# Performance work log

Measured on AMD Instinct MI355X. Metric: run time of the kernel, lower is better.

Reference implementation:

```python
import jax, jax.numpy as jnp
import numpy as np

N_NODES = 50000
N_EDGES = 800000
N_FEAT = 256
HIDDEN = 64
N_CLASSES = 16
T_END = 3.0  # opt['time']; rk4 takes one step over [0, 3]


def spline_conv(x, src, dst, p, W, R, b, n):
    """SplineConv, dim=1, kernel_size=2, degree=1 open B-spline, aggr='mean'.
    x: [n, Cin]; src/dst: [E]; p: [E,1] pseudo-coords in [0,1];
    W: [2, Cin, Cout]; R: [Cin, Cout]; b: [Cout]."""
    xj = x[src]  # gather source node features [E, Cin]
    # basis weights for K=2, degree=1: (1-p) on kernel 0, p on kernel 1
    msg = ((1.0 - p) * xj) @ W[0] + (p * xj) @ W[1]  # [E, Cout]
    agg = jax.ops.segment_sum(msg, dst, num_segments=n)
    deg = jax.ops.segment_sum(jnp.ones((msg.shape[0], 1), msg.dtype), dst, num_segments=n)
    return agg / jnp.maximum(deg, 1.0) + x @ R + b


def setup_inputs() -> dict:
    key = jax.random.key(0)
    ks = jax.random.split(key, 20)
    x = jax.random.normal(ks[0], (N_NODES, N_FEAT), jnp.float32)
    edge_attr = jax.random.uniform(ks[1], (N_EDGES, 1), jnp.float32)
    src = jax.random.randint(ks[2], (N_EDGES,), 0, N_NODES)
    dst = jax.random.randint(ks[3], (N_EDGES,), 0, N_NODES)

    def w(k, shape, fan_in):
        s = 1.0 / np.sqrt(fan_in)
        return jax.random.uniform(k, shape, jnp.float32, -s, s)

    # conv1: num_features -> hidden
    W1 = w(ks[4], (2, N_FEAT, HIDDEN), N_FEAT)
    R1 = w(ks[5], (N_FEAT, HIDDEN), N_FEAT)
    b1 = jnp.zeros((HIDDEN,), jnp.float32)
    # ODE func: two stacked SplineConvs hidden -> hidden
    Wa = w(ks[6], (2, HIDDEN, HIDDEN), HIDDEN)
    Ra = w(ks[7], (HIDDEN, HIDDEN), HIDDEN)
    ba = jnp.zeros((HIDDEN,), jnp.float32)
    Wb = w(ks[8], (2, HIDDEN, HIDDEN), HIDDEN)
    Rb = w(ks[9], (HIDDEN, HIDDEN), HIDDEN)
    bb = jnp.zeros((HIDDEN,), jnp.float32)
    # conv2: hidden -> num_classes
    W2 = w(ks[10], (2, HIDDEN, N_CLASSES), HIDDEN)
    R2 = w(ks[11], (HIDDEN, N_CLASSES), HIDDEN)
    b2 = jnp.zeros((N_CLASSES,), jnp.float32)

    return dict(x=x, edge_attr=edge_attr, src=src, dst=dst,
                W1=W1, R1=R1, b1=b1, Wa=Wa, Ra=Ra, ba=ba,
                Wb=Wb, Rb=Rb, bb=bb, W2=W2, R2=R2, b2=b2)


def reference(x, edge_attr, src, dst, W1, R1, b1, Wa, Ra, ba, Wb, Rb, bb, W2, R2, b2):
    n = x.shape[0]
    p = edge_attr
    h = jnp.tanh(spline_conv(x, src, dst, p, W1, R1, b1, n))
    # dropout is identity in eval mode

    def f(y):  # GCNLayer: two stacked SplineConvs, no activation
        y = spline_conv(y, src, dst, p, Wa, Ra, ba, n)
        return spline_conv(y, src, dst, p, Wb, Rb, bb, n)

    # single RK4 step from t=0 to t=T_END (torchdiffeq fixed-grid rk4 on s_span=[0,3])
    k1 = f(h)
    k2 = f(h + 0.5 * T_END * k1)
    k3 = f(h + 0.5 * T_END * k2)
    k4 = f(h + T_END * k3)
    h = h + (T_END / 6.0) * (k1 + 2.0 * k2 + 2.0 * k3 + k4)

    out = jnp.tanh(spline_conv(h, src, dst, p, W2, R2, b2, n))
    return jax.nn.log_softmax(out, axis=1)
```

## Files before the change

### kernel.cpp

```cpp
#include <hip/hip_runtime.h>
#include <math.h>

static inline int ceil_div(int a, int b) { return (a + b - 1) / b; }


__global__ __launch_bounds__(256) void zero2(int* __restrict__ a, int* __restrict__ b,
                                             int n) {
    int i = blockIdx.x * 256 + threadIdx.x;
    if (i < n) { a[i] = 0; b[i] = 0; }
}

__global__ __launch_bounds__(256) void hist_kernel(const int* __restrict__ dst,
                                                   int* __restrict__ deg, int E) {
    int e = blockIdx.x * 256 + threadIdx.x;
    if (e < E) atomicAdd(&deg[dst[e]], 1);
}

__global__ __launch_bounds__(256) void scan_blocksum(const int* __restrict__ deg,
                                                     int* __restrict__ bsum, int n) {
    __shared__ int red[256];
    int t = threadIdx.x;
    int base = blockIdx.x * 2048 + t * 8;
    int s = 0;
    #pragma unroll
    for (int i = 0; i < 8; ++i) {
        int idx = base + i;
        if (idx < n) s += deg[idx];
    }
    red[t] = s;
    __syncthreads();
    #pragma unroll
    for (int off = 128; off >= 1; off >>= 1) {
        if (t < off) red[t] += red[t + off];
        __syncthreads();
    }
    if (t == 0) bsum[blockIdx.x] = red[0];
}

__global__ __launch_bounds__(256) void scan_tops(int* __restrict__ bsum, int nb) {
    __shared__ int sh[256];
    int t = threadIdx.x;
    int orig = (t < nb) ? bsum[t] : 0;
    sh[t] = orig;
    __syncthreads();
    for (int off = 1; off < 256; off <<= 1) {
        int add = (t >= off) ? sh[t - off] : 0;
        __syncthreads();
        sh[t] += add;
        __syncthreads();
    }
    if (t < nb) bsum[t] = sh[t] - orig;
}

__global__ __launch_bounds__(256) void scan_final(const int* __restrict__ deg,
                                                  const int* __restrict__ bsum,
                                                  int* __restrict__ rowp,
                                                  float* __restrict__ invd,
                                                  int n, int E) {
    __shared__ int sh[256];
    int t = threadIdx.x;
    int base = blockIdx.x * 2048 + t * 8;
    int loc[8];
    int s = 0;
    #pragma unroll
    for (int i = 0; i < 8; ++i) {
        int idx = base + i;
        int d = (idx < n) ? deg[idx] : 0;
        loc[i] = d;
        s += d;
    }
    sh[t] = s;
    __syncthreads();
    for (int off = 1; off < 256; off <<= 1) {
        int add = (t >= off) ? sh[t - off] : 0;
        __syncthreads();
        sh[t] += add;
        __syncthreads();
    }
    int run = bsum[blockIdx.x] + (sh[t] - s);
    #pragma unroll
    for (int i = 0; i < 8; ++i) {
        int idx = base + i;
        if (idx < n) {
            rowp[idx] = run;
            int d = loc[i];
            run += d;
            invd[idx] = 1.0f / (float)(d > 1 ? d : 1);
        }
    }
    if (blockIdx.x == 0 && t == 0) rowp[n] = E;
}

__global__ __launch_bounds__(256) void scatter_idx(const int* __restrict__ dst,
                                                   const int* __restrict__ rowp,
                                                   int* __restrict__ fill,
                                                   int* __restrict__ ei, int E) {
    int e = blockIdx.x * 256 + threadIdx.x;
    if (e >= E) return;
    int d = dst[e];
    int pos = rowp[d] + atomicAdd(&fill[d], 1);
    ei[pos] = e;
}

__global__ __launch_bounds__(256) void sort_fill(const int* __restrict__ rowp,
                                                 int* __restrict__ ei,
                                                 const int* __restrict__ src,
                                                 const float* __restrict__ p,
                                                 int* __restrict__ es,
                                                 float* __restrict__ ep, int n) {
    int node = blockIdx.x * 256 + threadIdx.x;
    if (node >= n) return;
    int b = rowp[node], e = rowp[node + 1];
    for (int i = b + 1; i < e; ++i) {
        int key = ei[i];
        int j = i - 1;
        while (j >= b && ei[j] > key) { ei[j + 1] = ei[j]; --j; }
        ei[j + 1] = key;
    }
    for (int i = b; i < e; ++i) {
        int id = ei[i];
        es[i] = src[id];
        ep[i] = p[id];
    }
}

__global__ __launch_bounds__(256) void pack_all(
    const float* __restrict__ W1, const float* __restrict__ R1,
    const float* __restrict__ Wa, const float* __restrict__ Ra,
    const float* __restrict__ Wb, const float* __restrict__ Rb,
    const float* __restrict__ W2, const float* __restrict__ R2,
    float* __restrict__ Bc1, float* __restrict__ Bca,
    float* __restrict__ Bcb, float* __restrict__ Bc2) {
    int idx = blockIdx.x * 256 + threadIdx.x;
    const int S1 = 256 * 192, S2 = 192 * 64, S4 = 64 * 48;
    if (idx < S1) {
        int k = idx / 192, c = idx % 192;
        float v;
        if (c < 64)       v = W1[k * 64 + c];
        else if (c < 128) v = W1[256 * 64 + k * 64 + (c - 64)];
        else              v = R1[k * 64 + (c - 128)];
        Bc1[idx] = v;
        return;
    }
    idx -= S1;
    if (idx < S2) { Bca[idx] = (idx < 8192) ? Wa[idx] : Ra[idx - 8192]; return; }
    idx -= S2;
    if (idx < S2) { Bcb[idx] = (idx < 8192) ? Wb[idx] : Rb[idx - 8192]; return; }
    idx -= S2;
    if (idx < S4) {
        int k = idx / 48, c = idx % 48;
        float v;
        if (c < 16)      v = W2[k * 16 + c];
        else if (c < 32) v = W2[64 * 16 + k * 16 + (c - 16)];
        else             v = R2[k * 16 + (c - 32)];
        Bc2[idx] = v;
    }
}

__global__ __launch_bounds__(256) void conv1_gemm(const float* __restrict__ x,
                                                  const float* __restrict__ B,
                                                  int n, float* __restrict__ yz,
                                                  float* __restrict__ base,
                                                  const float* __restrict__ b1) {
    __shared__ __align__(16) float As[16][68];
    __shared__ __align__(16) float Bs[16][200];
    const int t = threadIdx.x;
    const int row0 = blockIdx.x * 64;
    const int ty = t >> 4, tx = t & 15;
    const int lrow = t >> 2, lk = (t & 3) << 2;
    const int bkk = t >> 4, bcol = (t & 15) << 2;
    float acc[4][12];
    #pragma unroll
    for (int i = 0; i < 4; ++i)
        #pragma unroll
        for (int j = 0; j < 12; ++j) acc[i][j] = 0.f;

    for (int k0 = 0; k0 < 256; k0 += 16) {
        float4 av = make_float4(0.f, 0.f, 0.f, 0.f);
        int r = row0 + lrow;
        if (r < n) av = *reinterpret_cast<const float4*>(&x[(size_t)r * 256 + k0 + lk]);
        As[lk + 0][lrow] = av.x; As[lk + 1][lrow] = av.y;
        As[lk + 2][lrow] = av.z; As[lk + 3][lrow] = av.w;
        const float* bp = &B[(size_t)(k0 + bkk) * 192 + bcol];
        *reinterpret_cast<float4*>(&Bs[bkk][bcol])       = *reinterpret_cast<const float4*>(bp);
        *reinterpret_cast<float4*>(&Bs[bkk][bcol + 64])  = *reinterpret_cast<const float4*>(bp + 64);
        *reinterpret_cast<float4*>(&Bs[bkk][bcol + 128]) = *reinterpret_cast<const float4*>(bp + 128);
        __syncthreads();
        #pragma unroll
        for (int kk = 0; kk < 16; ++kk) {
            float4 a4 = *reinterpret_cast<const float4*>(&As[kk][ty << 2]);
            float4 b0 = *reinterpret_cast<const float4*>(&Bs[kk][tx << 2]);
            float4 b1v = *reinterpret_cast<const float4*>(&Bs[kk][(tx << 2) + 64]);
            float4 b2v = *reinterpret_cast<const float4*>(&Bs[kk][(tx << 2) + 128]);
            float aa[4] = {a4.x, a4.y, a4.z, a4.w};
            float bb[12] = {b0.x, b0.y, b0.z, b0.w, b1v.x, b1v.y, b1v.z, b1v.w,
                            b2v.x, b2v.y, b2v.z, b2v.w};
            #pragma unroll
            for (int i = 0; i < 4; ++i)
                #pragma unroll
                for (int j = 0; j < 12; ++j)
                    acc[i][j] = fmaf(aa[i], bb[j], acc[i][j]);
        }
        __syncthreads();
    }

    float4 bb4 = *reinterpret_cast<const float4*>(&b1[tx << 2]);
    #pragma unroll
    for (int i = 0; i < 4; ++i) {
        int r = row0 + (ty << 2) + i;
        if (r >= n) continue;
        float4 q0 = make_float4(acc[i][0], acc[i][1], acc[i][2], acc[i][3]);
        float4 q1 = make_float4(acc[i][4], acc[i][5], acc[i][6], acc[i][7]);
        float4 q2 = make_float4(acc[i][8] + bb4.x, acc[i][9] + bb4.y,
                                acc[i][10] + bb4.z, acc[i][11] + bb4.w);
        *reinterpret_cast<float4*>(&yz[(size_t)r * 128 + (tx << 2)]) = q0;
        *reinterpret_cast<float4*>(&yz[(size_t)r * 128 + 64 + (tx << 2)]) = q1;
        *reinterpret_cast<float4*>(&base[(size_t)r * 64 + (tx << 2)]) = q2;
    }
}

__global__ __launch_bounds__(256) void hidden_fused(
    const float* __restrict__ in, const int* __restrict__ rowp,
    const int* __restrict__ es, const float* __restrict__ ep,
    const float* __restrict__ invd, const float* __restrict__ B,
    const float* __restrict__ bias, int n, int mode,
    float* __restrict__ u_out,
    const float* __restrict__ hbuf, const float* __restrict__ acc_in,
    float* __restrict__ acc_out, float* __restrict__ t_out,
    float c1, float c2, float c3) {
    __shared__ __align__(16) float As[192][68];
    __shared__ __align__(16) float Bs[16][68];
    const int t = threadIdx.x;
    const int row0 = blockIdx.x * 64;
    const int c4 = (t & 15) << 2;
    const int ng = t >> 4;

    for (int sub = 0; sub < 4; ++sub) {
        int nl = (sub << 4) + ng;
        int node = row0 + nl;
        if (node < n) {
            int e = rowp[node], eend = rowp[node + 1];
            float sx = 0.f, sy = 0.f, sz = 0.f, sw = 0.f;
            float px = 0.f, py = 0.f, pz = 0.f, pw = 0.f;
            for (; e + 4 <= eend; e += 4) {
                int a = es[e], b = es[e + 1], c = es[e + 2], d = es[e + 3];
                float pa = ep[e], pb = ep[e + 1], pc = ep[e + 2], pd = ep[e + 3];
                float4 va = *reinterpret_cast<const float4*>(&in[(size_t)a * 64 + c4]);
                float4 vb = *reinterpret_cast<const float4*>(&in[(size_t)b * 64 + c4]);
                float4 vc = *reinterpret_cast<const float4*>(&in[(size_t)c * 64 + c4]);
                float4 vd = *reinterpret_cast<const float4*>(&in[(size_t)d * 64 + c4]);
                sx += (va.x + vb.x) + (vc.x + vd.x);
                sy += (va.y + vb.y) + (vc.y + vd.y);
                sz += (va.z + vb.z) + (vc.z + vd.z);
                sw += (va.w + vb.w) + (vc.w + vd.w);
                px = fmaf(pa, va.x, fmaf(pb, vb.x, fmaf(pc, vc.x, fmaf(pd, vd.x, px))));
                py = fmaf(pa, va.y, fmaf(pb, vb.y, fmaf(pc, vc.y, fmaf(pd, vd.y, py))));
                pz = fmaf(pa, va.z, fmaf(pb, vb.z, fmaf(pc, vc.z, fmaf(pd, vd.z, pz))));
                pw = fmaf(pa, va.w, fmaf(pb, vb.w, fmaf(pc, vc.w, fmaf(pd, vd.w, pw))));
            }
            for (; e < eend; ++e) {
                int s = es[e];
                float pe = ep[e];
                float4 v = *reinterpret_cast<const float4*>(&in[(size_t)s * 64 + c4]);
                sx += v.x; sy += v.y; sz += v.z; sw += v.w;
                px = fmaf(pe, v.x, px); py = fmaf(pe, v.y, py);
                pz = fmaf(pe, v.z, pz); pw = fmaf(pe, v.w, pw);
            }
            float w = invd[node];
            float4 r4 = *reinterpret_cast<const float4*>(&in[(size_t)node * 64 + c4]);
            As[c4 + 0][nl] = (sx - px) * w;
            As[c4 + 1][nl] = (sy - py) * w;
            As[c4 + 2][nl] = (sz - pz) * w;
            As[c4 + 3][nl] = (sw - pw) * w;
            As[64 + c4 + 0][nl] = px * w;
            As[64 + c4 + 1][nl] = py * w;
            As[64 + c4 + 2][nl] = pz * w;
            As[64 + c4 + 3][nl] = pw * w;
            As[128 + c4 + 0][nl] = r4.x;
            As[128 + c4 + 1][nl] = r4.y;
            As[128 + c4 + 2][nl] = r4.z;
            As[128 + c4 + 3][nl] = r4.w;
        } else {
            #pragma unroll
            for (int i = 0; i < 4; ++i) {
                As[c4 + i][nl] = 0.f;
                As[64 + c4 + i][nl] = 0.f;
                As[128 + c4 + i][nl] = 0.f;
            }
        }
    }
    __syncthreads();

    const int ty = t >> 4, tx = t & 15;
    float acc[4][4];
    #pragma unroll
    for (int i = 0; i < 4; ++i)
        #pragma unroll
        for (int j = 0; j < 4; ++j) acc[i][j] = 0.f;

    for (int s = 0; s < 12; ++s) {
        *reinterpret_cast<float4*>(&Bs[t >> 4][(t & 15) << 2]) =
            *reinterpret_cast<const float4*>(&B[(size_t)((s << 4) + (t >> 4)) * 64 + ((t & 15) << 2)]);
        __syncthreads();
        #pragma unroll
        for (int kk = 0; kk < 16; ++kk) {
            float4 a4 = *reinterpret_cast<const float4*>(&As[(s << 4) + kk][ty << 2]);
            float4 b4 = *reinterpret_cast<const float4*>(&Bs[kk][tx << 2]);
            float aa[4] = {a4.x, a4.y, a4.z, a4.w};
            float bb[4] = {b4.x, b4.y, b4.z, b4.w};
            #pragma unroll
            for (int i = 0; i < 4; ++i)
                #pragma unroll
                for (int j = 0; j < 4; ++j)
                    acc[i][j] = fmaf(aa[i], bb[j], acc[i][j]);
        }
        __syncthreads();
    }

    float4 bv = *reinterpret_cast<const float4*>(&bias[tx << 2]);
    #pragma unroll
    for (int i = 0; i < 4; ++i) {
        int r = row0 + (ty << 2) + i;
        if (r >= n) continue;
        size_t idx = (size_t)r * 64 + (tx << 2);
        float4 v = make_float4(acc[i][0] + bv.x, acc[i][1] + bv.y,
                               acc[i][2] + bv.z, acc[i][3] + bv.w);
        if (mode == 0) {
            *reinterpret_cast<float4*>(&u_out[idx]) = v;
        } else {
            float4 ai = make_float4(0.f, 0.f, 0.f, 0.f);
            if (acc_in) ai = *reinterpret_cast<const float4*>(&acc_in[idx]);
            float4 an = make_float4(ai.x + c3 * v.x, ai.y + c3 * v.y,
                                    ai.z + c3 * v.z, ai.w + c3 * v.w);
            *reinterpret_cast<float4*>(&acc_out[idx]) = an;
            float4 hb = *reinterpret_cast<const float4*>(&hbuf[idx]);
            float4 to = make_float4(hb.x + c1 * v.x + c2 * an.x,
                                    hb.y + c1 * v.y + c2 * an.y,
                                    hb.z + c1 * v.z + c2 * an.z,
                                    hb.w + c1 * v.w + c2 * an.w);
            *reinterpret_cast<float4*>(&t_out[idx]) = to;
        }
    }
}


__global__ __launch_bounds__(256) void edge_tf64_v4(const float* __restrict__ yz,
                                                    const int* __restrict__ rowp,
                                                    const int* __restrict__ es,
                                                    const float* __restrict__ ep,
                                                    const float* __restrict__ invd,
                                                    const float* __restrict__ base,
                                                    float* __restrict__ out, int n) {
    int gid = blockIdx.x * 256 + threadIdx.x;
    int node = gid >> 4;
    if (node >= n) return;
    int c4 = (gid & 15) << 2;
    int e = rowp[node], eend = rowp[node + 1];
    float ax = 0.f, ay = 0.f, az = 0.f, aw = 0.f;
    for (; e + 2 <= eend; e += 2) {
        int s0 = es[e], s1 = es[e + 1];
        float p0 = ep[e], p1 = ep[e + 1];
        float4 y0 = *reinterpret_cast<const float4*>(&yz[(size_t)s0 * 128 + c4]);
        float4 z0 = *reinterpret_cast<const float4*>(&yz[(size_t)s0 * 128 + 64 + c4]);
        float4 y1 = *reinterpret_cast<const float4*>(&yz[(size_t)s1 * 128 + c4]);
        float4 z1 = *reinterpret_cast<const float4*>(&yz[(size_t)s1 * 128 + 64 + c4]);
        ax += fmaf(p0, z0.x - y0.x, y0.x) + fmaf(p1, z1.x - y1.x, y1.x);
        ay += fmaf(p0, z0.y - y0.y, y0.y) + fmaf(p1, z1.y - y1.y, y1.y);
        az += fmaf(p0, z0.z - y0.z, y0.z) + fmaf(p1, z1.z - y1.z, y1.z);
        aw += fmaf(p0, z0.w - y0.w, y0.w) + fmaf(p1, z1.w - y1.w, y1.w);
    }
    for (; e < eend; ++e) {
        int s = es[e];
        float pe = ep[e];
        float4 y = *reinterpret_cast<const float4*>(&yz[(size_t)s * 128 + c4]);
        float4 z = *reinterpret_cast<const float4*>(&yz[(size_t)s * 128 + 64 + c4]);
        ax += fmaf(pe, z.x - y.x, y.x);
        ay += fmaf(pe, z.y - y.y, y.y);
        az += fmaf(pe, z.z - y.z, y.z);
        aw += fmaf(pe, z.w - y.w, y.w);
    }
    float w = invd[node];
    size_t idx = (size_t)node * 64 + c4;
    float4 b = *reinterpret_cast<const float4*>(&base[idx]);
    float4 o = make_float4(tanhf(fmaf(ax, w, b.x)), tanhf(fmaf(ay, w, b.y)),
                           tanhf(fmaf(az, w, b.z)), tanhf(fmaf(aw, w, b.w)));
    *reinterpret_cast<float4*>(&out[idx]) = o;
}

__global__ __launch_bounds__(256) void edge_tf16_lsm(const float* __restrict__ yz,
                                                     const int* __restrict__ rowp,
                                                     const int* __restrict__ es,
                                                     const float* __restrict__ ep,
                                                     const float* __restrict__ invd,
                                                     const float* __restrict__ base,
                                                     float* __restrict__ out, int n) {
    int gid = blockIdx.x * 256 + threadIdx.x;
    int node = gid >> 4;
    if (node >= n) return;
    int c = gid & 15;
    int e = rowp[node], eend = rowp[node + 1];
    float a = 0.f;
    for (; e + 4 <= eend; e += 4) {
        int s0 = es[e], s1 = es[e + 1], s2 = es[e + 2], s3 = es[e + 3];
        float p0 = ep[e], p1 = ep[e + 1], p2 = ep[e + 2], p3 = ep[e + 3];
        float y0 = yz[(size_t)s0 * 32 + c],      z0 = yz[(size_t)s0 * 32 + 16 + c];
        float y1 = yz[(size_t)s1 * 32 + c],      z1 = yz[(size_t)s1 * 32 + 16 + c];
        float y2 = yz[(size_t)s2 * 32 + c],      z2 = yz[(size_t)s2 * 32 + 16 + c];
        float y3 = yz[(size_t)s3 * 32 + c],      z3 = yz[(size_t)s3 * 32 + 16 + c];
        a += fmaf(p0, z0 - y0, y0);
        a += fmaf(p1, z1 - y1, y1);
        a += fmaf(p2, z2 - y2, y2);
        a += fmaf(p3, z3 - y3, y3);
    }
    for (; e < eend; ++e) {
        int s = es[e]; float pe = ep[e];
        float y = yz[(size_t)s * 32 + c], z = yz[(size_t)s * 32 + 16 + c];
        a += fmaf(pe, z - y, y);
    }
    float o = tanhf(a * invd[node] + base[(size_t)node * 16 + c]);
    float m = o;
    #pragma unroll
    for (int off = 8; off >= 1; off >>= 1) m = fmaxf(m, __shfl_xor(m, off, 16));
    float ex = expf(o - m);
    float s = ex;
    #pragma unroll
    for (int off = 8; off >= 1; off >>= 1) s += __shfl_xor(s, off, 16);
    out[(size_t)node * 16 + c] = (o - m) - logf(s);
}

__global__ __launch_bounds__(256) void gemm_tiled(
    const float* __restrict__ A0, int lda0, int K0,
    const float* __restrict__ A1, int lda1,
    const float* __restrict__ B,
    int n, int K, int M,
    float* __restrict__ out0, int w0, const float* __restrict__ bias0,
    float* __restrict__ out1, int w1, const float* __restrict__ bias1,
    int split, int mode,
    const float* __restrict__ hbuf, const float* __restrict__ acc_in,
    float* __restrict__ acc_out, float* __restrict__ t_out,
    float c1, float c2, float c3) {
    __shared__ __align__(16) float As[16][68];
    __shared__ __align__(16) float Bs[16][68];
    const int t = threadIdx.x;
    const int row0 = blockIdx.x * 64;
    const int col0 = blockIdx.y * 64;
    const int ty = t >> 4, tx = t & 15;
    const int lrow = t >> 2, lk = (t & 3) << 2;
    const int bkk = t >> 4, bcol = (t & 15) << 2;
    float acc[4][4];
    #pragma unroll
    for (int i = 0; i < 4; ++i)
        #pragma unroll
        for (int j = 0; j < 4; ++j) acc[i][j] = 0.f;

    for (int k0 = 0; k0 < K; k0 += 16) {
        float4 av = make_float4(0.f, 0.f, 0.f, 0.f);
        {
            int r = row0 + lrow;
            if (r < n) {
                int kk = k0 + lk;
                const float* src = (kk < K0)
                    ? (A0 + (size_t)r * lda0 + kk)
                    : (A1 + (size_t)r * lda1 + (kk - K0));
                av = *reinterpret_cast<const float4*>(src);
            }
        }
        float4 bv = make_float4(0.f, 0.f, 0.f, 0.f);
        {
            int c = col0 + bcol;
            int kk = k0 + bkk;
            if (c < M) bv = *reinterpret_cast<const float4*>(B + (size_t)kk * M + c);
        }
        As[lk + 0][lrow] = av.x; As[lk + 1][lrow] = av.y;
        As[lk + 2][lrow] = av.z; As[lk + 3][lrow] = av.w;
        *reinterpret_cast<float4*>(&Bs[bkk][bcol]) = bv;
        __syncthreads();
        #pragma unroll
        for (int kk = 0; kk < 16; ++kk) {
            float4 a4 = *reinterpret_cast<const float4*>(&As[kk][ty << 2]);
            float4 b4 = *reinterpret_cast<const float4*>(&Bs[kk][tx << 2]);
            float aa[4] = {a4.x, a4.y, a4.z, a4.w};
            float bb[4] = {b4.x, b4.y, b4.z, b4.w};
            #pragma unroll
            for (int i = 0; i < 4; ++i)
                #pragma unroll
                for (int j = 0; j < 4; ++j)
                    acc[i][j] = fmaf(aa[i], bb[j], acc[i][j]);
        }
        __syncthreads();
    }

    #pragma unroll
    for (int i = 0; i < 4; ++i) {
        int r = row0 + (ty << 2) + i;
        if (r >= n) continue;
        #pragma unroll
        for (int j = 0; j < 4; ++j) {
            int c = col0 + (tx << 2) + j;
            if (c >= M) continue;
            float v = acc[i][j];
            if (c < split) {
                if (bias0) v += bias0[c];
                out0[(size_t)r * w0 + c] = v;
            } else {
                int cc = c - split;
                if (bias1) v += bias1[cc];
                out1[(size_t)r * w1 + cc] = v;
            }
        }
    }
}


extern "C" void kernel_launch(void* const* d_in, const int* in_sizes, int n_in,
                              void* d_out, int out_size, void* d_ws, size_t ws_size,
                              hipStream_t stream) {
    const float* x  = (const float*)d_in[0];
    const float* pE = (const float*)d_in[1];
    const int*   sr = (const int*)d_in[2];
    const int*   ds = (const int*)d_in[3];
    const float* W1 = (const float*)d_in[4];
    const float* R1 = (const float*)d_in[5];
    const float* b1 = (const float*)d_in[6];
    const float* Wa = (const float*)d_in[7];
    const float* Ra = (const float*)d_in[8];
    const float* ba = (const float*)d_in[9];
    const float* Wb = (const float*)d_in[10];
    const float* Rb = (const float*)d_in[11];
    const float* bb = (const float*)d_in[12];
    const float* W2 = (const float*)d_in[13];
    const float* R2 = (const float*)d_in[14];
    const float* b2 = (const float*)d_in[15];
    const int n = in_sizes[0] / 256;
    const int E = in_sizes[2];
    float* out = (float*)d_out;

    char* w = (char*)d_ws;
    auto alloc = [&](size_t bytes) -> void* {
        void* ptr = (void*)w;
        w += (bytes + 255) & ~(size_t)255;
        return ptr;
    };
    int nscan = ceil_div(n, 2048);
    int*   deg  = (int*)alloc((size_t)n * 4);
    int*   fill = (int*)alloc((size_t)n * 4);
    int*   rowp = (int*)alloc((size_t)(n + 1) * 4);
    float* invd = (float*)alloc((size_t)n * 4);
    int*   bsum = (int*)alloc((size_t)256 * 4);
    int*   ei   = (int*)alloc((size_t)E * 4);
    int*   es   = (int*)alloc((size_t)E * 4);
    float* ep   = (float*)alloc((size_t)E * 4);
    float* Bc1  = (float*)alloc((size_t)256 * 192 * 4);
    float* Bca  = (float*)alloc((size_t)192 * 64 * 4);
    float* Bcb  = (float*)alloc((size_t)192 * 64 * 4);
    float* Bc2  = (float*)alloc((size_t)64 * 48 * 4);
    float* big0 = (float*)alloc((size_t)n * 128 * 4);
    float* big1 = (float*)alloc((size_t)n * 64 * 4);
    float* h    = (float*)alloc((size_t)n * 64 * 4);
    float* u    = (float*)alloc((size_t)n * 64 * 4);
    float* tb   = (float*)alloc((size_t)n * 64 * 4);
    float* acc  = (float*)alloc((size_t)n * 64 * 4);

    const int PACK_TOTAL = 256 * 192 + 2 * 192 * 64 + 64 * 48;

    zero2<<<ceil_div(n, 256), 256, 0, stream>>>(deg, fill, n);
    pack_all<<<ceil_div(PACK_TOTAL, 256), 256, 0, stream>>>(W1, R1, Wa, Ra, Wb, Rb,
                                                            W2, R2, Bc1, Bca, Bcb, Bc2);
    hist_kernel<<<ceil_div(E, 256), 256, 0, stream>>>(ds, deg, E);
    scan_blocksum<<<nscan, 256, 0, stream>>>(deg, bsum, n);
    scan_tops<<<1, 256, 0, stream>>>(bsum, nscan);
    scan_final<<<nscan, 256, 0, stream>>>(deg, bsum, rowp, invd, n, E);
    scatter_idx<<<ceil_div(E, 256), 256, 0, stream>>>(ds, rowp, fill, ei, E);
    sort_fill<<<ceil_div(n, 256), 256, 0, stream>>>(rowp, ei, sr, pE, es, ep, n);

    const int gb = ceil_div(n, 64);

    conv1_gemm<<<gb, 256, 0, stream>>>(x, Bc1, n, big0, big1, b1);
    edge_tf64_v4<<<ceil_div(n * 16, 256), 256, 0, stream>>>(big0, rowp, es, ep, invd,
                                                            big1, h, n);

    hidden_fused<<<gb, 256, 0, stream>>>(h, rowp, es, ep, invd, Bca, ba, n, 0, u,
                                         nullptr, nullptr, nullptr, nullptr, 0.f, 0.f, 0.f);
    hidden_fused<<<gb, 256, 0, stream>>>(u, rowp, es, ep, invd, Bcb, bb, n, 1, nullptr,
                                         h, nullptr, acc, tb, 1.5f, 0.f, 1.f);
    hidden_fused<<<gb, 256, 0, stream>>>(tb, rowp, es, ep, invd, Bca, ba, n, 0, u,
                                         nullptr, nullptr, nullptr, nullptr, 0.f, 0.f, 0.f);
    hidden_fused<<<gb, 256, 0, stream>>>(u, rowp, es, ep, invd, Bcb, bb, n, 1, nullptr,
                                         h, acc, acc, tb, 1.5f, 0.f, 2.f);
    hidden_fused<<<gb, 256, 0, stream>>>(tb, rowp, es, ep, invd, Bca, ba, n, 0, u,
                                         nullptr, nullptr, nullptr, nullptr, 0.f, 0.f, 0.f);
    hidden_fused<<<gb, 256, 0, stream>>>(u, rowp, es, ep, invd, Bcb, bb, n, 1, nullptr,
                                         h, acc, acc, tb, 3.f, 0.f, 2.f);
    hidden_fused<<<gb, 256, 0, stream>>>(tb, rowp, es, ep, invd, Bca, ba, n, 0, u,
                                         nullptr, nullptr, nullptr, nullptr, 0.f, 0.f, 0.f);
    hidden_fused<<<gb, 256, 0, stream>>>(u, rowp, es, ep, invd, Bcb, bb, n, 1, nullptr,
                                         h, acc, acc, tb, 0.f, 0.5f, 1.f);

    {
        dim3 g(gb, 1);
        gemm_tiled<<<g, 256, 0, stream>>>(tb, 64, 64, nullptr, 0, Bc2, n, 64, 48,
                                          big0, 32, nullptr, big1, 16, b2, 32, 0,
                                          nullptr, nullptr, nullptr, nullptr, 0.f, 0.f, 0.f);
        edge_tf16_lsm<<<ceil_div(n * 16, 256), 256, 0, stream>>>(big0, rowp, es, ep, invd,
                                                                 big1, out, n);
    }
}
```

Measured before the change: 996.4 us.

## Split fused hidden conv into aggregation kernel plus double-buffered GEMM

Each hidden SplineConv previously ran as one fused kernel that gathered neighbours into a large 192x68 shared tile and then ran the GEMM. It is now split into an edge aggregation kernel that writes a 128-wide aggregate buffer to global memory, followed by a register-prefetched, double-buffered GEMM that reads that buffer plus the input. The goal is to drop the heavy shared-memory footprint so more blocks fit per CU and gathers get more parallelism. The cost is an extra global round trip of about 512 bytes per node per conv and twice as many launches. The conv1 GEMM also gains register-prefetch double buffering.

Result: faster. 926.0 us (-7.1%).

```diff
diff --git a/kernel.cpp b/kernel.cpp
--- a/kernel.cpp
+++ b/kernel.cpp
@@ -157,155 +157,99 @@
     }
 }
 
-__global__ __launch_bounds__(256) void conv1_gemm(const float* __restrict__ x,
-                                                  const float* __restrict__ B,
-                                                  int n, float* __restrict__ yz,
-                                                  float* __restrict__ base,
-                                                  const float* __restrict__ b1) {
-    __shared__ __align__(16) float As[16][68];
-    __shared__ __align__(16) float Bs[16][200];
+__global__ __launch_bounds__(256) void edge_agg64_v4(const float* __restrict__ x,
+                                                     const int* __restrict__ rowp,
+                                                     const int* __restrict__ es,
+                                                     const float* __restrict__ ep,
+                                                     const float* __restrict__ invd,
+                                                     float* __restrict__ agg, int n) {
+    int gid = blockIdx.x * 256 + threadIdx.x;
+    int node = gid >> 4;
+    if (node >= n) return;
+    int c4 = (gid & 15) << 2;
+    int e = rowp[node], eend = rowp[node + 1];
+    float sx = 0.f, sy = 0.f, sz = 0.f, sw = 0.f;
+    float px = 0.f, py = 0.f, pz = 0.f, pw = 0.f;
+    for (; e + 4 <= eend; e += 4) {
+        int s0 = es[e], s1 = es[e + 1], s2 = es[e + 2], s3 = es[e + 3];
+        float p0 = ep[e], p1 = ep[e + 1], p2 = ep[e + 2], p3 = ep[e + 3];
+        float4 v0 = *reinterpret_cast<const float4*>(&x[(size_t)s0 * 64 + c4]);
+        float4 v1 = *reinterpret_cast<const float4*>(&x[(size_t)s1 * 64 + c4]);
+        float4 v2 = *reinterpret_cast<const float4*>(&x[(size_t)s2 * 64 + c4]);
+        float4 v3 = *reinterpret_cast<const float4*>(&x[(size_t)s3 * 64 + c4]);
+        sx += (v0.x + v1.x) + (v2.x + v3.x);
+        sy += (v0.y + v1.y) + (v2.y + v3.y);
+        sz += (v0.z + v1.z) + (v2.z + v3.z);
+        sw += (v0.w + v1.w) + (v2.w + v3.w);
+        px = fmaf(p0, v0.x, fmaf(p1, v1.x, fmaf(p2, v2.x, fmaf(p3, v3.x, px))));
+        py = fmaf(p0, v0.y, fmaf(p1, v1.y, fmaf(p2, v2.y, fmaf(p3, v3.y, py))));
+        pz = fmaf(p0, v0.z, fmaf(p1, v1.z, fmaf(p2, v2.z, fmaf(p3, v3.z, pz))));
+        pw = fmaf(p0, v0.w, fmaf(p1, v1.w, fmaf(p2, v2.w, fmaf(p3, v3.w, pw))));
+    }
+    for (; e < eend; ++e) {
+        int s = es[e];
+        float pe = ep[e];
+        float4 v = *reinterpret_cast<const float4*>(&x[(size_t)s * 64 + c4]);
+        sx += v.x; sy += v.y; sz += v.z; sw += v.w;
+        px = fmaf(pe, v.x, px); py = fmaf(pe, v.y, py);
+        pz = fmaf(pe, v.z, pz); pw = fmaf(pe, v.w, pw);
+    }
+    float w = invd[node];
+    float4 a0 = make_float4((sx - px) * w, (sy - py) * w, (sz - pz) * w, (sw - pw) * w);
+    float4 a1 = make_float4(px * w, py * w, pz * w, pw * w);
+    *reinterpret_cast<float4*>(&agg[(size_t)node * 128 + c4]) = a0;
+    *reinterpret_cast<float4*>(&agg[(size_t)node * 128 + 64 + c4]) = a1;
+}
+
+__global__ __launch_bounds__(256) void hidden_gemm_db(
+    const float* __restrict__ agg, const float* __restrict__ in,
+    const float* __restrict__ B, const float* __restrict__ bias,
+    int n, int mode, float* __restrict__ u_out,
+    const float* __restrict__ hbuf, const float* __restrict__ acc_in,
+    float* __restrict__ acc_out, float* __restrict__ t_out,
+    float c1, float c2, float c3) {
+    __shared__ __align__(16) float As[2][16][68];
+    __shared__ __align__(16) float Bs[2][16][68];
     const int t = threadIdx.x;
     const int row0 = blockIdx.x * 64;
     const int ty = t >> 4, tx = t & 15;
     const int lrow = t >> 2, lk = (t & 3) << 2;
     const int bkk = t >> 4, bcol = (t & 15) << 2;
-    float acc[4][12];
-    #pragma unroll
-    for (int i = 0; i < 4; ++i)
-        #pragma unroll
-        for (int j = 0; j < 12; ++j) acc[i][j] = 0.f;
-
-    for (int k0 = 0; k0 < 256; k0 += 16) {
-        float4 av = make_float4(0.f, 0.f, 0.f, 0.f);
+
+    float4 av = make_float4(0.f, 0.f, 0.f, 0.f);
+    {
         int r = row0 + lrow;
-        if (r < n) av = *reinterpret_cast<const float4*>(&x[(size_t)r * 256 + k0 + lk]);
-        As[lk + 0][lrow] = av.x; As[lk + 1][lrow] = av.y;
-        As[lk + 2][lrow] = av.z; As[lk + 3][lrow] = av.w;
-        const float* bp = &B[(size_t)(k0 + bkk) * 192 + bcol];
-        *reinterpret_cast<float4*>(&Bs[bkk][bcol])       = *reinterpret_cast<const float4*>(bp);
-        *reinterpret_cast<float4*>(&Bs[bkk][bcol + 64])  = *reinterpret_cast<const float4*>(bp + 64);
-        *reinterpret_cast<float4*>(&Bs[bkk][bcol + 128]) = *reinterpret_cast<const float4*>(bp + 128);
-        __syncthreads();
-        #pragma unroll
-        for (int kk = 0; kk < 16; ++kk) {
-            float4 a4 = *reinterpret_cast<const float4*>(&As[kk][ty << 2]);
-            float4 b0 = *reinterpret_cast<const float4*>(&Bs[kk][tx << 2]);
-            float4 b1v = *reinterpret_cast<const float4*>(&Bs[kk][(tx << 2) + 64]);
-            float4 b2v = *reinterpret_cast<const float4*>(&Bs[kk][(tx << 2) + 128]);
-            float aa[4] = {a4.x, a4.y, a4.z, a4.w};
-            float bb[12] = {b0.x, b0.y, b0.z, b0.w, b1v.x, b1v.y, b1v.z, b1v.w,
-                            b2v.x, b2v.y, b2v.z, b2v.w};
-            #pragma unroll
-            for (int i = 0; i < 4; ++i)
-                #pragma unroll
-                for (int j = 0; j < 12; ++j)
-                    acc[i][j] = fmaf(aa[i], bb[j], acc[i][j]);
-        }
-        __syncthreads();
-    }
-
-    float4 bb4 = *reinterpret_cast<const float4*>(&b1[tx << 2]);
-    #pragma unroll
-    for (int i = 0; i < 4; ++i) {
-        int r = row0 + (ty << 2) + i;
-        if (r >= n) continue;
-        float4 q0 = make_float4(acc[i][0], acc[i][1], acc[i][2], acc[i][3]);
-        float4 q1 = make_float4(acc[i][4], acc[i][5], acc[i][6], acc[i][7]);
-        float4 q2 = make_float4(acc[i][8] + bb4.x, acc[i][9] + bb4.y,
-                                acc[i][10] + bb4.z, acc[i][11] + bb4.w);
-        *reinterpret_cast<float4*>(&yz[(size_t)r * 128 + (tx << 2)]) = q0;
-        *reinterpret_cast<float4*>(&yz[(size_t)r * 128 + 64 + (tx << 2)]) = q1;
-        *reinterpret_cast<float4*>(&base[(size_t)r * 64 + (tx << 2)]) = q2;
-    }
-}
-
-__global__ __launch_bounds__(256) void hidden_fused(
-    const float* __restrict__ in, const int* __restrict__ rowp,
-    const int* __restrict__ es, const float* __restrict__ ep,
-    const float* __restrict__ invd, const float* __restrict__ B,
-    const float* __restrict__ bias, int n, int mode,
-    float* __restrict__ u_out,
-    const float* __restrict__ hbuf, const float* __restrict__ acc_in,
-    float* __restrict__ acc_out, float* __restrict__ t_out,
-    float c1, float c2, float c3) {
-    __shared__ __align__(16) float As[192][68];
-    __shared__ __align__(16) float Bs[16][68];
-    const int t = threadIdx.x;
-    const int row0 = blockIdx.x * 64;
-    const int c4 = (t & 15) << 2;
-    const int ng = t >> 4;
-
-    for (int sub = 0; sub < 4; ++sub) {
-        int nl = (sub << 4) + ng;
-        int node = row0 + nl;
-        if (node < n) {
-            int e = rowp[node], eend = rowp[node + 1];
-            float sx = 0.f, sy = 0.f, sz = 0.f, sw = 0.f;
-            float px = 0.f, py = 0.f, pz = 0.f, pw = 0.f;
-            for (; e + 4 <= eend; e += 4) {
-                int a = es[e], b = es[e + 1], c = es[e + 2], d = es[e + 3];
-                float pa = ep[e], pb = ep[e + 1], pc = ep[e + 2], pd = ep[e + 3];
-                float4 va = *reinterpret_cast<const float4*>(&in[(size_t)a * 64 + c4]);
-                float4 vb = *reinterpret_cast<const float4*>(&in[(size_t)b * 64 + c4]);
-                float4 vc = *reinterpret_cast<const float4*>(&in[(size_t)c * 64 + c4]);
-                float4 vd = *reinterpret_cast<const float4*>(&in[(size_t)d * 64 + c4]);
-                sx += (va.x + vb.x) + (vc.x + vd.x);
-                sy += (va.y + vb.y) + (vc.y + vd.y);
-                sz += (va.z + vb.z) + (vc.z + vd.z);
-                sw += (va.w + vb.w) + (vc.w + vd.w);
-                px = fmaf(pa, va.x, fmaf(pb, vb.x, fmaf(pc, vc.x, fmaf(pd, vd.x, px))));
-                py = fmaf(pa, va.y, fmaf(pb, vb.y, fmaf(pc, vc.y, fmaf(pd, vd.y, py))));
-                pz = fmaf(pa, va.z, fmaf(pb, vb.z, fmaf(pc, vc.z, fmaf(pd, vd.z, pz))));
-                pw = fmaf(pa, va.w, fmaf(pb, vb.w, fmaf(pc, vc.w, fmaf(pd, vd.w, pw))));
-            }
-            for (; e < eend; ++e) {
-                int s = es[e];
-                float pe = ep[e];
-                float4 v = *reinterpret_cast<const float4*>(&in[(size_t)s * 64 + c4]);
-                sx += v.x; sy += v.y; sz += v.z; sw += v.w;
-                px = fmaf(pe, v.x, px); py = fmaf(pe, v.y, py);
-                pz = fmaf(pe, v.z, pz); pw = fmaf(pe, v.w, pw);
-            }
-            float w = invd[node];
-            float4 r4 = *reinterpret_cast<const float4*>(&in[(size_t)node * 64 + c4]);
-            As[c4 + 0][nl] = (sx - px) * w;
-            As[c4 + 1][nl] = (sy - py) * w;
-            As[c4 + 2][nl] = (sz - pz) * w;
-            As[c4 + 3][nl] = (sw - pw) * w;
-            As[64 + c4 + 0][nl] = px * w;
-            As[64 + c4 + 1][nl] = py * w;
-            As[64 + c4 + 2][nl] = pz * w;
-            As[64 + c4 + 3][nl] = pw * w;
-            As[128 + c4 + 0][nl] = r4.x;
-            As[128 + c4 + 1][nl] = r4.y;
-            As[128 + c4 + 2][nl] = r4.z;
-            As[128 + c4 + 3][nl] = r4.w;
-        } else {
-            #pragma unroll
-            for (int i = 0; i < 4; ++i) {
-                As[c4 + i][nl] = 0.f;
-                As[64 + c4 + i][nl] = 0.f;
-                As[128 + c4 + i][nl] = 0.f;
-            }
-        }
-    }
+        if (r < n) av = *reinterpret_cast<const float4*>(&agg[(size_t)r * 128 + lk]);
+    }
+    float4 bv = *reinterpret_cast<const float4*>(&B[(size_t)bkk * 64 + bcol]);
+    As[0][lk + 0][lrow] = av.x; As[0][lk + 1][lrow] = av.y;
+    As[0][lk + 2][lrow] = av.z; As[0][lk + 3][lrow] = av.w;
+    *reinterpret_cast<float4*>(&Bs[0][bkk][bcol]) = bv;
     __syncthreads();
 
-    const int ty = t >> 4, tx = t & 15;
     float acc[4][4];
     #pragma unroll
     for (int i = 0; i < 4; ++i)
         #pragma unroll
         for (int j = 0; j < 4; ++j) acc[i][j] = 0.f;
 
-    for (int s = 0; s < 12; ++s) {
-        *reinterpret_cast<float4*>(&Bs[t >> 4][(t & 15) << 2]) =
-            *reinterpret_cast<const float4*>(&B[(size_t)((s << 4) + (t >> 4)) * 64 + ((t & 15) << 2)]);
-        __syncthreads();
+    for (int kt = 0; kt < 12; ++kt) {
+        const int cur = kt & 1;
+        if (kt + 1 < 12) {
+            int k0 = (kt + 1) << 4;
+            int r = row0 + lrow;
+            int kk = k0 + lk;
+            av = make_float4(0.f, 0.f, 0.f, 0.f);
+            if (r < n)
+                av = (kk < 128)
+                    ? *reinterpret_cast<const float4*>(&agg[(size_t)r * 128 + kk])
+                    : *reinterpret_cast<const float4*>(&in[(size_t)r * 64 + (kk - 128)]);
+            bv = *reinterpret_cast<const float4*>(&B[(size_t)(k0 + bkk) * 64 + bcol]);
+        }
         #pragma unroll
         for (int kk = 0; kk < 16; ++kk) {
-            float4 a4 = *reinterpret_cast<const float4*>(&As[(s << 4) + kk][ty << 2]);
-            float4 b4 = *reinterpret_cast<const float4*>(&Bs[kk][tx << 2]);
+            float4 a4 = *reinterpret_cast<const float4*>(&As[cur][kk][ty << 2]);
+            float4 b4 = *reinterpret_cast<const float4*>(&Bs[cur][kk][tx << 2]);
             float aa[4] = {a4.x, a4.y, a4.z, a4.w};
             float bb[4] = {b4.x, b4.y, b4.z, b4.w};
             #pragma unroll
@@ -314,17 +258,23 @@
                 for (int j = 0; j < 4; ++j)
                     acc[i][j] = fmaf(aa[i], bb[j], acc[i][j]);
         }
-        __syncthreads();
-    }
-
-    float4 bv = *reinterpret_cast<const float4*>(&bias[tx << 2]);
+        if (kt + 1 < 12) {
+            const int nx = cur ^ 1;
+            As[nx][lk + 0][lrow] = av.x; As[nx][lk + 1][lrow] = av.y;
+            As[nx][lk + 2][lrow] = av.z; As[nx][lk + 3][lrow] = av.w;
+            *reinterpret_cast<float4*>(&Bs[nx][bkk][bcol]) = bv;
+        }
+        __syncthreads();
+    }
+
+    float4 bia = *reinterpret_cast<const float4*>(&bias[tx << 2]);
     #pragma unroll
     for (int i = 0; i < 4; ++i) {
         int r = row0 + (ty << 2) + i;
         if (r >= n) continue;
         size_t idx = (size_t)r * 64 + (tx << 2);
-        float4 v = make_float4(acc[i][0] + bv.x, acc[i][1] + bv.y,
-                               acc[i][2] + bv.z, acc[i][3] + bv.w);
+        float4 v = make_float4(acc[i][0] + bia.x, acc[i][1] + bia.y,
+                               acc[i][2] + bia.z, acc[i][3] + bia.w);
         if (mode == 0) {
             *reinterpret_cast<float4*>(&u_out[idx]) = v;
         } else {
@@ -340,6 +290,95 @@
                                     hb.w + c1 * v.w + c2 * an.w);
             *reinterpret_cast<float4*>(&t_out[idx]) = to;
         }
+    }
+}
+
+__global__ __launch_bounds__(256) void conv1_gemm_db(const float* __restrict__ x,
+                                                     const float* __restrict__ B,
+                                                     int n, float* __restrict__ yz,
+                                                     float* __restrict__ base,
+                                                     const float* __restrict__ b1) {
+    __shared__ __align__(16) float As[2][16][68];
+    __shared__ __align__(16) float Bs[2][16][200];
+    const int t = threadIdx.x;
+    const int row0 = blockIdx.x * 64;
+    const int ty = t >> 4, tx = t & 15;
+    const int lrow = t >> 2, lk = (t & 3) << 2;
+    const int bkk = t >> 4, bcol = (t & 15) << 2;
+
+    float4 av = make_float4(0.f, 0.f, 0.f, 0.f);
+    {
+        int r = row0 + lrow;
+        if (r < n) av = *reinterpret_cast<const float4*>(&x[(size_t)r * 256 + lk]);
+    }
+    const float* bp0 = &B[(size_t)bkk * 192 + bcol];
+    float4 bv0 = *reinterpret_cast<const float4*>(bp0);
+    float4 bv1 = *reinterpret_cast<const float4*>(bp0 + 64);
+    float4 bv2 = *reinterpret_cast<const float4*>(bp0 + 128);
+    As[0][lk + 0][lrow] = av.x; As[0][lk + 1][lrow] = av.y;
+    As[0][lk + 2][lrow] = av.z; As[0][lk + 3][lrow] = av.w;
+    *reinterpret_cast<float4*>(&Bs[0][bkk][bcol]) = bv0;
+    *reinterpret_cast<float4*>(&Bs[0][bkk][bcol + 64]) = bv1;
+    *reinterpret_cast<float4*>(&Bs[0][bkk][bcol + 128]) = bv2;
+    __syncthreads();
+
+    float acc[4][12];
+    #pragma unroll
+    for (int i = 0; i < 4; ++i)
+        #pragma unroll
+        for (int j = 0; j < 12; ++j) acc[i][j] = 0.f;
+
+    for (int kt = 0; kt < 16; ++kt) {
+        const int cur = kt & 1;
+        if (kt + 1 < 16) {
+            int k0 = (kt + 1) << 4;
+            int r = row0 + lrow;
+            av = make_float4(0.f, 0.f, 0.f, 0.f);
+            if (r < n)
+                av = *reinterpret_cast<const float4*>(&x[(size_t)r * 256 + k0 + lk]);
+            const float* bp = &B[(size_t)(k0 + bkk) * 192 + bcol];
+            bv0 = *reinterpret_cast<const float4*>(bp);
+            bv1 = *reinterpret_cast<const float4*>(bp + 64);
+            bv2 = *reinterpret_cast<const float4*>(bp + 128);
+        }
+        #pragma unroll
+        for (int kk = 0; kk < 16; ++kk) {
+            float4 a4 = *reinterpret_cast<const float4*>(&As[cur][kk][ty << 2]);
+            float4 b0 = *reinterpret_cast<const float4*>(&Bs[cur][kk][tx << 2]);
+            float4 b1v = *reinterpret_cast<const float4*>(&Bs[cur][kk][(tx << 2) + 64]);
+            float4 b2v = *reinterpret_cast<const float4*>(&Bs[cur][kk][(tx << 2) + 128]);
+            float aa[4] = {a4.x, a4.y, a4.z, a4.w};
+            float bb[12] = {b0.x, b0.y, b0.z, b0.w, b1v.x, b1v.y, b1v.z, b1v.w,
+                            b2v.x, b2v.y, b2v.z, b2v.w};
+            #pragma unroll
+            for (int i = 0; i < 4; ++i)
+                #pragma unroll
+                for (int j = 0; j < 12; ++j)
+                    acc[i][j] = fmaf(aa[i], bb[j], acc[i][j]);
+        }
+        if (kt + 1 < 16) {
+            const int nx = cur ^ 1;
+            As[nx][lk + 0][lrow] = av.x; As[nx][lk + 1][lrow] = av.y;
+            As[nx][lk + 2][lrow] = av.z; As[nx][lk + 3][lrow] = av.w;
+            *reinterpret_cast<float4*>(&Bs[nx][bkk][bcol]) = bv0;
+            *reinterpret_cast<float4*>(&Bs[nx][bkk][bcol + 64]) = bv1;
+            *reinterpret_cast<float4*>(&Bs[nx][bkk][bcol + 128]) = bv2;
+        }
+        __syncthreads();
+    }
+
+    float4 bb4 = *reinterpret_cast<const float4*>(&b1[tx << 2]);
+    #pragma unroll
+    for (int i = 0; i < 4; ++i) {
+        int r = row0 + (ty << 2) + i;
+        if (r >= n) continue;
+        float4 q0 = make_float4(acc[i][0], acc[i][1], acc[i][2], acc[i][3]);
+        float4 q1 = make_float4(acc[i][4], acc[i][5], acc[i][6], acc[i][7]);
+        float4 q2 = make_float4(acc[i][8] + bb4.x, acc[i][9] + bb4.y,
+                                acc[i][10] + bb4.z, acc[i][11] + bb4.w);
+        *reinterpret_cast<float4*>(&yz[(size_t)r * 128 + (tx << 2)]) = q0;
+        *reinterpret_cast<float4*>(&yz[(size_t)r * 128 + 64 + (tx << 2)]) = q1;
+        *reinterpret_cast<float4*>(&base[(size_t)r * 64 + (tx << 2)]) = q2;
     }
 }
 
@@ -435,10 +474,7 @@
     int n, int K, int M,
     float* __restrict__ out0, int w0, const float* __restrict__ bias0,
     float* __restrict__ out1, int w1, const float* __restrict__ bias1,
-    int split, int mode,
-    const float* __restrict__ hbuf, const float* __restrict__ acc_in,
-    float* __restrict__ acc_out, float* __restrict__ t_out,
-    float c1, float c2, float c3) {
+    int split) {
     __shared__ __align__(16) float As[16][68];
     __shared__ __align__(16) float Bs[16][68];
     const int t = threadIdx.x;
@@ -511,6 +547,19 @@
     }
 }
 
+
+static void hidden_conv(hipStream_t stream, const float* in, float* agg,
+                        const int* rowp, const int* es, const float* ep,
+                        const float* invd, const float* Bc, const float* bias, int n,
+                        int mode, float* u_out,
+                        const float* h, const float* acc_in, float* acc_out,
+                        float* t_out, float c1, float c2, float c3) {
+    edge_agg64_v4<<<ceil_div(n * 16, 256), 256, 0, stream>>>(in, rowp, es, ep, invd,
+                                                             agg, n);
+    hidden_gemm_db<<<ceil_div(n, 64), 256, 0, stream>>>(agg, in, Bc, bias, n, mode,
+                                                        u_out, h, acc_in, acc_out,
+                                                        t_out, c1, c2, c3);
+}
 
 extern "C" void kernel_launch(void* const* d_in, const int* in_sizes, int n_in,
                               void* d_out, int out_size, void* d_ws, size_t ws_size,
@@ -575,33 +624,29 @@
 
     const int gb = ceil_div(n, 64);
 
-    conv1_gemm<<<gb, 256, 0, stream>>>(x, Bc1, n, big0, big1, b1);
+    conv1_gemm_db<<<gb, 256, 0, stream>>>(x, Bc1, n, big0, big1, b1);
     edge_tf64_v4<<<ceil_div(n * 16, 256), 256, 0, stream>>>(big0, rowp, es, ep, invd,
                                                             big1, h, n);
 
-    hidden_fused<<<gb, 256, 0, stream>>>(h, rowp, es, ep, invd, Bca, ba, n, 0, u,
-                                         nullptr, nullptr, nullptr, nullptr, 0.f, 0.f, 0.f);
-    hidden_fused<<<gb, 256, 0, stream>>>(u, rowp, es, ep, invd, Bcb, bb, n, 1, nullptr,
-                                         h, nullptr, acc, tb, 1.5f, 0.f, 1.f);
-    hidden_fused<<<gb, 256, 0, stream>>>(tb, rowp, es, ep, invd, Bca, ba, n, 0, u,
-                                         nullptr, nullptr, nullptr, nullptr, 0.f, 0.f, 0.f);
-    hidden_fused<<<gb, 256, 0, stream>>>(u, rowp, es, ep, invd, Bcb, bb, n, 1, nullptr,
-                                         h, acc, acc, tb, 1.5f, 0.f, 2.f);
-    hidden_fused<<<gb, 256, 0, stream>>>(tb, rowp, es, ep, invd, Bca, ba, n, 0, u,
-                                         nullptr, nullptr, nullptr, nullptr, 0.f, 0.f, 0.f);
-    hidden_fused<<<gb, 256, 0, stream>>>(u, rowp, es, ep, invd, Bcb, bb, n, 1, nullptr,
-                                         h, acc, acc, tb, 3.f, 0.f, 2.f);
-    hidden_fused<<<gb, 256, 0, stream>>>(tb, rowp, es, ep, invd, Bca, ba, n, 0, u,
-                                         nullptr, nullptr, nullptr, nullptr, 0.f, 0.f, 0.f);
-    hidden_fused<<<gb, 256, 0, stream>>>(u, rowp, es, ep, invd, Bcb, bb, n, 1, nullptr,
-                                         h, acc, acc, tb, 0.f, 0.5f, 1.f);
-
-    {
-        dim3 g(gb, 1);
-        gemm_tiled<<<g, 256, 0, stream>>>(tb, 64, 64, nullptr, 0, Bc2, n, 64, 48,
-                                          big0, 32, nullptr, big1, 16, b2, 32, 0,
-                                          nullptr, nullptr, nullptr, nullptr, 0.f, 0.f, 0.f);
-        edge_tf16_lsm<<<ceil_div(n * 16, 256), 256, 0, stream>>>(big0, rowp, es, ep, invd,
-                                                                 big1, out, n);
-    }
-}
+    hidden_conv(stream, h, big0, rowp, es, ep, invd, Bca, ba, n, 0, u,
+                nullptr, nullptr, nullptr, nullptr, 0.f, 0.f, 0.f);
+    hidden_conv(stream, u, big0, rowp, es, ep, invd, Bcb, bb, n, 1, nullptr,
+                h, nullptr, acc, tb, 1.5f, 0.f, 1.f);
+    hidden_conv(stream, tb, big0, rowp, es, ep, invd, Bca, ba, n, 0, u,
+                nullptr, nullptr, nullptr, nullptr, 0.f, 0.f, 0.f);
+    hidden_conv(stream, u, big0, rowp, es, ep, invd, Bcb, bb, n, 1, nullptr,
+                h, acc, acc, tb, 1.5f, 0.f, 2.f);
+    hidden_conv(stream, tb, big0, rowp, es, ep, invd, Bca, ba, n, 0, u,
+                nullptr, nullptr, nullptr, nullptr, 0.f, 0.f, 0.f);
+    hidden_conv(stream, u, big0, rowp, es, ep, invd, Bcb, bb, n, 1, nullptr,
+                h, acc, acc, tb, 3.f, 0.f, 2.f);
+    hidden_conv(stream, tb, big0, rowp, es, ep, invd, Bca, ba, n, 0, u,
+                nullptr, nullptr, nullptr, nullptr, 0.f, 0.f, 0.f);
+    hidden_conv(stream, u, big0, rowp, es, ep, invd, Bcb, bb, n, 1, nullptr,
+                h, acc, acc, tb, 0.f, 0.5f, 1.f);
+
+    gemm_tiled<<<dim3(gb, 1), 256, 0, stream>>>(tb, 64, 64, nullptr, 0, Bc2, n, 64, 48,
+                                                big0, 32, nullptr, big1, 16, b2, 32);
+    edge_tf16_lsm<<<ceil_div(n * 16, 256), 256, 0, stream>>>(big0, rowp, es, ep, invd,
+                                                             big1, out, n);
+}
```
